# Optimization experiments

Measured on AMD Instinct MI355X. Metric: run time of the kernel, lower is better.

Reference implementation:

```python
import jax, jax.numpy as jnp
import numpy as np

N = 200000   # num nodes
E = 2500000  # num edges
H = 32       # hidden_dim
EPS = 1e-5   # BatchNorm eps


def _gcn_conv(x, W, b, src, dst, norm):
    # GCNConv: D^{-1/2}(A+I)D^{-1/2} X W + b  (self-loops folded in via norm^2 term)
    h = x @ W                                   # [N, H_out]
    coef = norm[src] * norm[dst]                # [E]
    msg = h[src] * coef[:, None]                # [E, H_out] -- dominant HBM traffic
    agg = jax.ops.segment_sum(msg, dst, num_segments=N)
    agg = agg + h * (norm * norm)[:, None]      # self-loop contribution
    return agg + b


def _bn(x, gamma, beta):
    # BatchNorm1d in training mode: batch statistics over the node dimension
    m = jnp.mean(x, axis=0)
    v = jnp.var(x, axis=0)
    return gamma * (x - m) * jax.lax.rsqrt(v + EPS) + beta


def setup_inputs() -> dict:
    key = jax.random.key(0)
    ks = jax.random.split(key, 12)
    x = jax.random.uniform(ks[0], (N, 1), dtype=jnp.float32) * 50.0  # degree-like feature
    edge_index = jax.random.randint(ks[1], (2, E), 0, N, dtype=jnp.int64)
    edge_attr = jax.random.normal(ks[2], (E,), dtype=jnp.float32)
    s = 0.1
    return {
        'x': x, 'edge_index': edge_index, 'edge_attr': edge_attr,
        'W1': jax.random.normal(ks[3], (1, H), dtype=jnp.float32) * s,
        'b1': jnp.zeros((H,), jnp.float32),
        'g1': jnp.ones((H,), jnp.float32), 'be1': jnp.zeros((H,), jnp.float32),
        'W2': jax.random.normal(ks[4], (H, H), dtype=jnp.float32) * s,
        'b2': jnp.zeros((H,), jnp.float32),
        'g2': jnp.ones((H,), jnp.float32), 'be2': jnp.zeros((H,), jnp.float32),
        'W3': jax.random.normal(ks[5], (H, H), dtype=jnp.float32) * s,
        'b3': jnp.zeros((H,), jnp.float32),
        'g3': jnp.ones((H,), jnp.float32), 'be3': jnp.zeros((H,), jnp.float32),
        'fcW': jax.random.normal(ks[6], (H, 1), dtype=jnp.float32) * s,
        'fcb': jnp.zeros((1,), jnp.float32),
    }


def reference(x, edge_index, edge_attr, W1, b1, g1, be1, W2, b2, g2, be2,
              W3, b3, g3, be3, fcW, fcb):
    src, dst = edge_index[0], edge_index[1]
    # symmetric normalization from degrees of A + I
    deg = jax.ops.segment_sum(jnp.ones((E,), x.dtype), dst, num_segments=N) + 1.0
    norm = jax.lax.rsqrt(deg)                   # deg^{-1/2}, [N]

    h = jax.nn.relu(_bn(_gcn_conv(x, W1, b1, src, dst, norm), g1, be1))
    h = jax.nn.relu(_bn(_gcn_conv(h, W2, b2, src, dst, norm), g2, be2))
    h = jax.nn.relu(_bn(_gcn_conv(h, W3, b3, src, dst, norm), g3, be3))
    # dropout is identity in eval / deterministic reference
    return h @ fcW + fcb                        # [N, 1]
```

## Files before the change

### kernel.cpp

```cpp
#include <hip/hip_runtime.h>
#include <hip/hip_bf16.h>
#include <hip/hip_fp16.h>

#define N_NODES 200000
#define N_EDGES 2500000
#define HID 32
#define BN_EPS 1e-5f

#define BKT_SHIFT 10
#define B_BKT ((N_NODES + 1023) / 1024)
#define PAD 16
#define CAPB 14336
#define EDGES_PER_BLK 8192
#define NB_SCAT ((N_EDGES + EDGES_PER_BLK - 1) / EDGES_PER_BLK)

#define SBANK 4096
#define SSTR 16
#define S1SUM 0
#define S1SQ  16
#define L2SUM 32
#define L2SQ  544
#define L3SUM 1056
#define L3SQ  1568

#define NBN32 6250
#define NBH   3125

typedef float nfloat4 __attribute__((ext_vector_type(4)));

__device__ __forceinline__ void atomAddF(float* p, float v) {
    unsafeAtomicAdd(p, v);
}

__device__ __forceinline__ void ntStore4(float* p, float a, float b, float c, float d) {
    nfloat4 v = {a, b, c, d};
    __builtin_nontemporal_store(v, (nfloat4*)p);
}

__global__ void k_init(int* __restrict__ bcur16, float* __restrict__ stats) {
    int i = blockIdx.x * blockDim.x + threadIdx.x;
    if (i < B_BKT * PAD) bcur16[i] = 0;
    if (i < 4 * SBANK) stats[i] = 0.0f;
}

__global__ void __launch_bounds__(1024)
k_scatter(const int* __restrict__ ei, int* __restrict__ bcur16,
          unsigned int* __restrict__ ebuf) {
    __shared__ int lh[B_BKT], lbase[B_BKT], lc[B_BKT];
    int t = threadIdx.x;
    if (t < B_BKT) { lh[t] = 0; lc[t] = 0; }
    __syncthreads();
    int base = blockIdx.x * EDGES_PER_BLK;
    int sv[8], dv[8];
#pragma unroll
    for (int k = 0; k < 8; k++) {
        int e = base + k * 1024 + t;
        if (e < N_EDGES) {
            sv[k] = ei[e];
            dv[k] = ei[N_EDGES + e];
            atomicAdd(&lh[dv[k] >> BKT_SHIFT], 1);
        } else dv[k] = -1;
    }
    __syncthreads();
    if (t < B_BKT) lbase[t] = lh[t] ? atomicAdd(&bcur16[t * PAD], lh[t]) : 0;
    __syncthreads();
#pragma unroll
    for (int k = 0; k < 8; k++) {
        if (dv[k] >= 0) {
            int b = dv[k] >> BKT_SHIFT;
            int loc = atomicAdd(&lc[b], 1);
            ebuf[(size_t)b * CAPB + lbase[b] + loc] =
                ((unsigned)(dv[k] & 1023) << 18) | (unsigned)sv[k];
        }
    }
}

__global__ void __launch_bounds__(1024)
k_bucket(const unsigned int* __restrict__ ebuf, const int* __restrict__ bcur16,
         const float* __restrict__ x, int* __restrict__ rowbeg,
         int* __restrict__ cntg, float* __restrict__ norm,
         float* __restrict__ xp, int* __restrict__ csrc) {
    __shared__ int hist[1024], rbase[1024];
    __shared__ int wsum[16];
    int b = blockIdx.x;
    int t = threadIdx.x;
    int lane = t & 63, wv = t >> 6;
    int count = bcur16[b * PAD];
    size_t ebase = (size_t)b * CAPB;
    int nbase = b << BKT_SHIFT;
    hist[t] = 0;
    __syncthreads();
    for (int i = t; i < count; i += 1024)
        atomicAdd(&hist[ebuf[ebase + i] >> 18], 1);
    __syncthreads();
    int v = hist[t];
    int val = v;
#pragma unroll
    for (int off = 1; off < 64; off <<= 1) {
        int nn = __shfl_up(val, off);
        if (lane >= off) val += nn;
    }
    if (lane == 63) wsum[wv] = val;
    __syncthreads();
    if (t < 16) {
        int wval = wsum[t];
        int wincl = wval;
#pragma unroll
        for (int off = 1; off < 16; off <<= 1) {
            int nn = __shfl_up(wincl, off, 16);
            if (t >= off) wincl += nn;
        }
        wsum[t] = wincl - wval;
    }
    __syncthreads();
    int excl = (val - v) + wsum[wv];
    int rb = b * CAPB + excl;
    rbase[t] = rb;
    int n = nbase + t;
    if (n < N_NODES) {
        rowbeg[n] = rb;
        cntg[n] = v;
        float nm = rsqrtf((float)v + 1.0f);
        norm[n] = nm;
        xp[n] = x[n] * nm;
    }
    __syncthreads();
    hist[t] = 0;
    __syncthreads();
    for (int i = t; i < count; i += 1024) {
        unsigned int w = ebuf[ebase + i];
        int ld = w >> 18;
        int loc = atomicAdd(&hist[ld], 1);
        csrc[rbase[ld] + loc] = (int)(w & 0x3FFFFu);
    }
}

__global__ void __launch_bounds__(256)
k_gather1(const int* __restrict__ rowbeg, const int* __restrict__ cntg,
          const int* __restrict__ csrc, const float* __restrict__ xp,
          const float* __restrict__ norm, float2* __restrict__ sn2,
          float* __restrict__ stats) {
    __shared__ float ls[256], lq[256];
    int tid = threadIdx.x;
    int nl = tid >> 3, q = tid & 7;
    int n = blockIdx.x * 32 + nl;
    int beg = rowbeg[n], dg = cntg[n];
    float A0 = 0.f, A1 = 0.f;
    int i = q;
    for (; i + 8 < dg; i += 16) {
        A0 += xp[__builtin_nontemporal_load(csrc + beg + i)];
        A1 += xp[__builtin_nontemporal_load(csrc + beg + i + 8)];
    }
    if (i < dg) A0 += xp[__builtin_nontemporal_load(csrc + beg + i)];
    float acc = A0 + A1;
    acc += __shfl_xor(acc, 1);
    acc += __shfl_xor(acc, 2);
    acc += __shfl_xor(acc, 4);
    float val = 0.f;
    if (q == 0) {
        acc += xp[n];
        float nm = norm[n];
        val = nm * acc;
        sn2[n] = make_float2(val, nm);
    }
    ls[tid] = val; lq[tid] = val * val;
    __syncthreads();
    for (int off = 128; off; off >>= 1) {
        if (tid < (unsigned)off) { ls[tid] += ls[tid + off]; lq[tid] += lq[tid + off]; }
        __syncthreads();
    }
    if (tid == 0) {
        int bo = (blockIdx.x & 3) * SBANK;
        atomAddF(&stats[bo + S1SUM], ls[0]);
        atomAddF(&stats[bo + S1SQ],  lq[0]);
    }
}

__global__ void __launch_bounds__(256)
k_layer2(const int* __restrict__ rowbeg, const int* __restrict__ cntg,
         const int* __restrict__ csrc, const float2* __restrict__ sn2,
         const float* __restrict__ stats, const float* __restrict__ W1,
         const float* __restrict__ g1, const float* __restrict__ be1,
         const float* __restrict__ W2, float* __restrict__ B,
         float* __restrict__ sumO, float* __restrict__ sqO) {
    __shared__ float w2s[1024];
    __shared__ __align__(16) float ajs[32], bjs[32];
    __shared__ float yx[32][36];
    __shared__ float red[4][8][8];
    int tid = threadIdx.x;
    for (int i = tid; i < 1024; i += 256) w2s[i] = W2[i];
    if (tid < 32) {
        float sm = stats[S1SUM] + stats[SBANK + S1SUM] +
                   stats[2*SBANK + S1SUM] + stats[3*SBANK + S1SUM];
        float sq = stats[S1SQ] + stats[SBANK + S1SQ] +
                   stats[2*SBANK + S1SQ] + stats[3*SBANK + S1SQ];
        float m   = sm * (1.0f / N_NODES);
        float var = sq * (1.0f / N_NODES) - m * m;
        float w = W1[tid];
        float a = g1[tid] * w * rsqrtf(var * w * w + BN_EPS);
        ajs[tid] = a;
        bjs[tid] = be1[tid] - m * a;
    }
    __syncthreads();
    int nl = tid >> 3, l = tid & 7, cg = l * 4;
    int n = blockIdx.x * 32 + nl;
    int dg = cntg[n];
    int beg = rowbeg[n];
    float2 self = sn2[n];
    float nm = self.y;
    float h[32];
#pragma unroll
    for (int k = 0; k < 32; k++) h[k] = 0.f;
    if (l == 0) {
#pragma unroll
        for (int k4 = 0; k4 < 32; k4 += 4) {
            float4 a4 = *(const float4*)&ajs[k4];
            float4 b4 = *(const float4*)&bjs[k4];
            h[k4+0] = nm * fmaxf(fmaf(a4.x, self.x, b4.x), 0.f);
            h[k4+1] = nm * fmaxf(fmaf(a4.y, self.x, b4.y), 0.f);
            h[k4+2] = nm * fmaxf(fmaf(a4.z, self.x, b4.z), 0.f);
            h[k4+3] = nm * fmaxf(fmaf(a4.w, self.x, b4.w), 0.f);
        }
    }
    for (int i = l; i < dg; i += 8) {
        float2 p = sn2[__builtin_nontemporal_load(csrc + beg + i)];
        float w = p.y;
#pragma unroll
        for (int k4 = 0; k4 < 32; k4 += 4) {
            float4 a4 = *(const float4*)&ajs[k4];
            float4 b4 = *(const float4*)&bjs[k4];
            h[k4+0] = fmaf(fmaxf(fmaf(a4.x, p.x, b4.x), 0.f), w, h[k4+0]);
            h[k4+1] = fmaf(fmaxf(fmaf(a4.y, p.x, b4.y), 0.f), w, h[k4+1]);
            h[k4+2] = fmaf(fmaxf(fmaf(a4.z, p.x, b4.z), 0.f), w, h[k4+2]);
            h[k4+3] = fmaf(fmaxf(fmaf(a4.w, p.x, b4.w), 0.f), w, h[k4+3]);
        }
    }
#pragma unroll
    for (int k = 0; k < 32; k++) {
        h[k] += __shfl_xor(h[k], 1);
        h[k] += __shfl_xor(h[k], 2);
        h[k] += __shfl_xor(h[k], 4);
    }
    *(float4*)&yx[nl][cg] = make_float4(h[cg], h[cg+1], h[cg+2], h[cg+3]);
    __syncthreads();
    float o0=0,o1=0,o2=0,o3=0;
#pragma unroll
    for (int k = 0; k < 32; k += 4) {
        float4 hh  = *(const float4*)&yx[nl][k];
        float4 wr0 = *(const float4*)&w2s[(k+0)*32 + cg];
        float4 wr1 = *(const float4*)&w2s[(k+1)*32 + cg];
        float4 wr2 = *(const float4*)&w2s[(k+2)*32 + cg];
        float4 wr3 = *(const float4*)&w2s[(k+3)*32 + cg];
        o0 = fmaf(hh.x,wr0.x, fmaf(hh.y,wr1.x, fmaf(hh.z,wr2.x, fmaf(hh.w,wr3.x, o0))));
        o1 = fmaf(hh.x,wr0.y, fmaf(hh.y,wr1.y, fmaf(hh.z,wr2.y, fmaf(hh.w,wr3.y, o1))));
        o2 = fmaf(hh.x,wr0.z, fmaf(hh.y,wr1.z, fmaf(hh.z,wr2.z, fmaf(hh.w,wr3.z, o2))));
        o3 = fmaf(hh.x,wr0.w, fmaf(hh.y,wr1.w, fmaf(hh.z,wr2.w, fmaf(hh.w,wr3.w, o3))));
    }
    o0 *= nm; o1 *= nm; o2 *= nm; o3 *= nm;
    ntStore4(B + (size_t)n * 32 + cg, o0, o1, o2, o3);
    float s0 = o0, s1 = o1, s2 = o2, s3 = o3;
    float q0 = o0*o0, q1 = o1*o1, q2 = o2*o2, q3 = o3*o3;
#pragma unroll
    for (int mask = 32; mask >= 8; mask >>= 1) {
        s0 += __shfl_xor(s0, mask); s1 += __shfl_xor(s1, mask);
        s2 += __shfl_xor(s2, mask); s3 += __shfl_xor(s3, mask);
        q0 += __shfl_xor(q0, mask); q1 += __shfl_xor(q1, mask);
        q2 += __shfl_xor(q2, mask); q3 += __shfl_xor(q3, mask);
    }
    int wv = tid >> 6, ln = tid & 63;
    if (ln < 8) {
        float* r = red[wv][ln];
        r[0]=s0; r[1]=s1; r[2]=s2; r[3]=s3;
        r[4]=q0; r[5]=q1; r[6]=q2; r[7]=q3;
    }
    __syncthreads();
    if (tid < 8) {
        float tacc[8] = {0,0,0,0,0,0,0,0};
#pragma unroll
        for (int w = 0; w < 4; w++)
#pragma unroll
            for (int k = 0; k < 8; k++) tacc[k] += red[w][tid][k];
        int cb = tid * 4;
        int bo = (blockIdx.x & 3) * SBANK;
#pragma unroll
        for (int k = 0; k < 4; k++) {
            atomAddF(&sumO[bo + (cb + k) * SSTR], tacc[k]);
            atomAddF(&sqO [bo + (cb + k) * SSTR], tacc[4 + k]);
        }
    }
}

__global__ void __launch_bounds__(256)
k_fusedB(const float* __restrict__ norm, const float* __restrict__ sum,
         const float* __restrict__ sumsq, const float* __restrict__ g,
         const float* __restrict__ be, const float* __restrict__ W,
         const float* __restrict__ aggIn, __half* __restrict__ hOut) {
    __shared__ float wl[1024];
    __shared__ float scs[32], shs[32];
    __shared__ float yx[32][36];
    int tid = threadIdx.x;
    for (int i = tid; i < 1024; i += 256) wl[i] = W[i];
    if (tid < 32) {
        int o = tid * SSTR;
        float sm = sum[o] + sum[o+SBANK] + sum[o+2*SBANK] + sum[o+3*SBANK];
        float sq = sumsq[o] + sumsq[o+SBANK] + sumsq[o+2*SBANK] + sumsq[o+3*SBANK];
        float m   = sm * (1.0f / N_NODES);
        float var = sq * (1.0f / N_NODES) - m * m;
        float scj = g[tid] * rsqrtf(var + BN_EPS);
        scs[tid] = scj;
        shs[tid] = be[tid] - m * scj;
    }
    __syncthreads();
    int nl = tid >> 3, cg = (tid & 7) * 4;
    int n = blockIdx.x * 32 + nl;
    float4 bi = *(const float4*)(aggIn + (size_t)n * 32 + cg);
    float y0 = fmaxf(scs[cg  ]*bi.x + shs[cg  ], 0.f);
    float y1 = fmaxf(scs[cg+1]*bi.y + shs[cg+1], 0.f);
    float y2 = fmaxf(scs[cg+2]*bi.z + shs[cg+2], 0.f);
    float y3 = fmaxf(scs[cg+3]*bi.w + shs[cg+3], 0.f);
    *(float4*)&yx[nl][cg] = make_float4(y0,y1,y2,y3);
    __syncthreads();
    float o0=0,o1=0,o2=0,o3=0;
#pragma unroll
    for (int k = 0; k < 32; k += 4) {
        float4 hh  = *(const float4*)&yx[nl][k];
        float4 wr0 = *(const float4*)&wl[(k+0)*32 + cg];
        float4 wr1 = *(const float4*)&wl[(k+1)*32 + cg];
        float4 wr2 = *(const float4*)&wl[(k+2)*32 + cg];
        float4 wr3 = *(const float4*)&wl[(k+3)*32 + cg];
        o0 = fmaf(hh.x,wr0.x, fmaf(hh.y,wr1.x, fmaf(hh.z,wr2.x, fmaf(hh.w,wr3.x, o0))));
        o1 = fmaf(hh.x,wr0.y, fmaf(hh.y,wr1.y, fmaf(hh.z,wr2.y, fmaf(hh.w,wr3.y, o1))));
        o2 = fmaf(hh.x,wr0.z, fmaf(hh.y,wr1.z, fmaf(hh.z,wr2.z, fmaf(hh.w,wr3.z, o2))));
        o3 = fmaf(hh.x,wr0.w, fmaf(hh.y,wr1.w, fmaf(hh.z,wr2.w, fmaf(hh.w,wr3.w, o3))));
    }
    float nm = norm[n];
    __half2 ha = __floats2half2_rn(o0 * nm, o1 * nm);
    __half2 hb = __floats2half2_rn(o2 * nm, o3 * nm);
    float2 pk;
    ((__half2*)&pk)[0] = ha;
    ((__half2*)&pk)[1] = hb;
    *(float2*)(hOut + (size_t)n * 32 + cg) = pk;
}

__device__ __forceinline__ void acc8(float* a, float4 raw) {
    const __half2* h = (const __half2*)&raw;
    float2 f0 = __half22float2(h[0]);
    float2 f1 = __half22float2(h[1]);
    float2 f2 = __half22float2(h[2]);
    float2 f3 = __half22float2(h[3]);
    a[0] += f0.x; a[1] += f0.y; a[2] += f1.x; a[3] += f1.y;
    a[4] += f2.x; a[5] += f2.y; a[6] += f3.x; a[7] += f3.y;
}

__device__ __forceinline__ void acc8m(float* a, float4 raw, float m) {
    const __half2* h = (const __half2*)&raw;
    float2 f0 = __half22float2(h[0]);
    float2 f1 = __half22float2(h[1]);
    float2 f2 = __half22float2(h[2]);
    float2 f3 = __half22float2(h[3]);
    a[0] = fmaf(m, f0.x, a[0]); a[1] = fmaf(m, f0.y, a[1]);
    a[2] = fmaf(m, f1.x, a[2]); a[3] = fmaf(m, f1.y, a[3]);
    a[4] = fmaf(m, f2.x, a[4]); a[5] = fmaf(m, f2.y, a[5]);
    a[6] = fmaf(m, f3.x, a[6]); a[7] = fmaf(m, f3.y, a[7]);
}

__global__ void __launch_bounds__(256)
k_gatherH(const int* __restrict__ rowbeg, const int* __restrict__ cntg,
          const int* __restrict__ csrc, const __half* __restrict__ A,
          const float* __restrict__ norm, float* __restrict__ B,
          float* __restrict__ sum, float* __restrict__ sumsq) {
    int tid = threadIdx.x;
    int nl = tid >> 2;
    int c8 = (tid & 3) * 8;
    int n = blockIdx.x * 64 + nl;
    int beg = rowbeg[n], dg = cntg[n];
    const __half* Ac = A + c8;
    float acc[8] = {0,0,0,0,0,0,0,0};
    acc8(acc, *(const float4*)(Ac + (size_t)n * 32));
    int iters = (dg + 7) >> 3;
    for (int t = 0; t < iters; t++) {
        int i0 = t * 8;
        int e[8]; float m[8];
#pragma unroll
        for (int j = 0; j < 8; j++) {
            int idx = i0 + j;
            bool ok = idx < dg;
            int ic = ok ? idx : dg - 1;
            e[j] = __builtin_nontemporal_load(csrc + beg + ic);
            m[j] = ok ? 1.f : 0.f;
        }
        float4 r0 = *(const float4*)(Ac + (size_t)e[0] * 32);
        float4 r1 = *(const float4*)(Ac + (size_t)e[1] * 32);
        float4 r2 = *(const float4*)(Ac + (size_t)e[2] * 32);
        float4 r3 = *(const float4*)(Ac + (size_t)e[3] * 32);
        float4 r4 = *(const float4*)(Ac + (size_t)e[4] * 32);
        float4 r5 = *(const float4*)(Ac + (size_t)e[5] * 32);
        float4 r6 = *(const float4*)(Ac + (size_t)e[6] * 32);
        float4 r7 = *(const float4*)(Ac + (size_t)e[7] * 32);
        acc8m(acc, r0, m[0]); acc8m(acc, r1, m[1]);
        acc8m(acc, r2, m[2]); acc8m(acc, r3, m[3]);
        acc8m(acc, r4, m[4]); acc8m(acc, r5, m[5]);
        acc8m(acc, r6, m[6]); acc8m(acc, r7, m[7]);
    }
    float nm = norm[n];
    float o[8];
#pragma unroll
    for (int k = 0; k < 8; k++) o[k] = acc[k] * nm;
    ntStore4(B + (size_t)n * 32 + c8,     o[0], o[1], o[2], o[3]);
    ntStore4(B + (size_t)n * 32 + c8 + 4, o[4], o[5], o[6], o[7]);
    float st[16];
#pragma unroll
    for (int k = 0; k < 8; k++) { st[k] = o[k]; st[8 + k] = o[k] * o[k]; }
#pragma unroll
    for (int mask = 32; mask >= 4; mask >>= 1)
#pragma unroll
        for (int k = 0; k < 16; k++) st[k] += __shfl_xor(st[k], mask);
    __shared__ float red[4][4][16];
    int wv = tid >> 6, ln = tid & 63;
    if (ln < 4) {
#pragma unroll
        for (int k = 0; k < 16; k++) red[wv][ln][k] = st[k];
    }
    __syncthreads();
    if (tid < 4) {
        float tacc[16];
#pragma unroll
        for (int k = 0; k < 16; k++) tacc[k] = 0.f;
#pragma unroll
        for (int w = 0; w < 4; w++)
#pragma unroll
            for (int k = 0; k < 16; k++) tacc[k] += red[w][tid][k];
        int cb = tid * 8;
        int bo = (blockIdx.x & 3) * SBANK;
#pragma unroll
        for (int k = 0; k < 8; k++) {
            atomAddF(&sum[bo + (cb + k) * SSTR], tacc[k]);
            atomAddF(&sumsq[bo + (cb + k) * SSTR], tacc[8 + k]);
        }
    }
}

__global__ void __launch_bounds__(256)
k_final(const float* __restrict__ aggIn, const float* __restrict__ sum,
        const float* __restrict__ sumsq, const float* __restrict__ g,
        const float* __restrict__ be, const float* __restrict__ fcW,
        const float* __restrict__ fcb, float* __restrict__ out) {
    __shared__ float scs[32], shs[32], fws[32];
    int tid = threadIdx.x;
    if (tid < 32) {
        int o = tid * SSTR;
        float sm = sum[o] + sum[o+SBANK] + sum[o+2*SBANK] + sum[o+3*SBANK];
        float sq = sumsq[o] + sumsq[o+SBANK] + sumsq[o+2*SBANK] + sumsq[o+3*SBANK];
        float m   = sm * (1.0f / N_NODES);
        float var = sq * (1.0f / N_NODES) - m * m;
        float scj = g[tid] * rsqrtf(var + BN_EPS);
        scs[tid] = scj;
        shs[tid] = be[tid] - m * scj;
        fws[tid] = fcW[tid];
    }
    __syncthreads();
    int nl = tid >> 3, cg = (tid & 7) * 4;
    int n = blockIdx.x * 32 + nl;
    float4 bi = *(const float4*)(aggIn + (size_t)n * 32 + cg);
    float v = fmaxf(scs[cg  ]*bi.x + shs[cg  ], 0.f) * fws[cg  ]
            + fmaxf(scs[cg+1]*bi.y + shs[cg+1], 0.f) * fws[cg+1]
            + fmaxf(scs[cg+2]*bi.z + shs[cg+2], 0.f) * fws[cg+2]
            + fmaxf(scs[cg+3]*bi.w + shs[cg+3], 0.f) * fws[cg+3];
    v += __shfl_xor(v, 1);
    v += __shfl_xor(v, 2);
    v += __shfl_xor(v, 4);
    if ((tid & 7) == 0) out[n] = v + fcb[0];
}

extern "C" void kernel_launch(void* const* d_in, const int* in_sizes, int n_in,
                              void* d_out, int out_size, void* d_ws, size_t ws_size,
                              hipStream_t stream) {
    const float* x   = (const float*)d_in[0];
    const int*   ei  = (const int*)d_in[1];
    const float* W1  = (const float*)d_in[3];
    const float* g1  = (const float*)d_in[5];
    const float* be1 = (const float*)d_in[6];
    const float* W2  = (const float*)d_in[7];
    const float* g2  = (const float*)d_in[9];
    const float* be2 = (const float*)d_in[10];
    const float* W3  = (const float*)d_in[11];
    const float* g3  = (const float*)d_in[13];
    const float* be3 = (const float*)d_in[14];
    const float* fcW = (const float*)d_in[15];
    const float* fcb = (const float*)d_in[16];
    float* out = (float*)d_out;

    char* base = (char*)d_ws;
    __half*       A16  = (__half*)base;
    unsigned int* ebuf = (unsigned int*)base;
    float*  B      = (float*)(base + (size_t)N_NODES * 32 * 4);
    int*    csrc   = (int*)(base + (size_t)N_NODES * 32 * 8);
    int*    rowbeg = csrc + (size_t)B_BKT * CAPB;
    int*    cntg   = rowbeg + N_NODES;
    float*  norm   = (float*)(cntg + N_NODES);
    float*  xp     = norm + N_NODES;
    float2* sn2    = (float2*)(xp + N_NODES);
    float*  stats  = (float*)(sn2 + N_NODES);
    int*    bcur16 = (int*)(stats + 4 * SBANK);

    k_init   <<<64, 256, 0, stream>>>(bcur16, stats);
    k_scatter<<<NB_SCAT, 1024, 0, stream>>>(ei, bcur16, ebuf);
    k_bucket <<<B_BKT, 1024, 0, stream>>>(ebuf, bcur16, x, rowbeg, cntg, norm, xp, csrc);
    k_gather1<<<NBN32, 256, 0, stream>>>(rowbeg, cntg, csrc, xp, norm, sn2, stats);
    k_layer2 <<<NBN32, 256, 0, stream>>>(rowbeg, cntg, csrc, sn2, stats,
                                         W1, g1, be1, W2, B,
                                         stats + L2SUM, stats + L2SQ);
    k_fusedB <<<NBN32, 256, 0, stream>>>(norm, stats + L2SUM, stats + L2SQ,
                                         g2, be2, W3, B, A16);
    k_gatherH<<<NBH, 256, 0, stream>>>(rowbeg, cntg, csrc, A16, norm, B,
                                       stats + L3SUM, stats + L3SQ);
    k_final  <<<NBN32, 256, 0, stream>>>(B, stats + L3SUM, stats + L3SQ,
                                         g3, be3, fcW, fcb, out);
}
```

Measured before the change: 346.0 us.

## Split layer-2 gather by channel instead of by edge, removing shuffle reduction

The layer-2 aggregation changes from each of 8 lanes handling a strided subset of edges for all 32 channels (then reducing with 96 shuffles) to each lane handling all edges for its own 4 channels. Each lane loads 8 edge indices and their sn2 entries per iteration. This drops the 32-register accumulator array and the cross-lane shuffle reduction, which should lower register pressure and ALU work. In exchange, every lane of the group now loads the same indices and sn2 values redundantly (broadcast loads), and the compute per lane is 4 channels times every edge.

```diff
diff --git a/kernel.cpp b/kernel.cpp
--- a/kernel.cpp
+++ b/kernel.cpp
@@ -175,6 +175,8 @@
         atomAddF(&stats[bo + S1SQ],  lq[0]);
     }
 }
+
+#define PHI(aa, bb, pp) ((pp).y * fmaxf(fmaf((aa), (pp).x, (bb)), 0.f))
 
 __global__ void __launch_bounds__(256)
 k_layer2(const int* __restrict__ rowbeg, const int* __restrict__ cntg,
@@ -202,46 +204,38 @@
         bjs[tid] = be1[tid] - m * a;
     }
     __syncthreads();
-    int nl = tid >> 3, l = tid & 7, cg = l * 4;
+    int nl = tid >> 3, cg = (tid & 7) * 4;
     int n = blockIdx.x * 32 + nl;
     int dg = cntg[n];
     int beg = rowbeg[n];
+    float a0 = ajs[cg], a1 = ajs[cg+1], a2 = ajs[cg+2], a3 = ajs[cg+3];
+    float b0 = bjs[cg], b1 = bjs[cg+1], b2 = bjs[cg+2], b3 = bjs[cg+3];
     float2 self = sn2[n];
     float nm = self.y;
-    float h[32];
-#pragma unroll
-    for (int k = 0; k < 32; k++) h[k] = 0.f;
-    if (l == 0) {
-#pragma unroll
-        for (int k4 = 0; k4 < 32; k4 += 4) {
-            float4 a4 = *(const float4*)&ajs[k4];
-            float4 b4 = *(const float4*)&bjs[k4];
-            h[k4+0] = nm * fmaxf(fmaf(a4.x, self.x, b4.x), 0.f);
-            h[k4+1] = nm * fmaxf(fmaf(a4.y, self.x, b4.y), 0.f);
-            h[k4+2] = nm * fmaxf(fmaf(a4.z, self.x, b4.z), 0.f);
-            h[k4+3] = nm * fmaxf(fmaf(a4.w, self.x, b4.w), 0.f);
-        }
-    }
-    for (int i = l; i < dg; i += 8) {
-        float2 p = sn2[__builtin_nontemporal_load(csrc + beg + i)];
-        float w = p.y;
-#pragma unroll
-        for (int k4 = 0; k4 < 32; k4 += 4) {
-            float4 a4 = *(const float4*)&ajs[k4];
-            float4 b4 = *(const float4*)&bjs[k4];
-            h[k4+0] = fmaf(fmaxf(fmaf(a4.x, p.x, b4.x), 0.f), w, h[k4+0]);
-            h[k4+1] = fmaf(fmaxf(fmaf(a4.y, p.x, b4.y), 0.f), w, h[k4+1]);
-            h[k4+2] = fmaf(fmaxf(fmaf(a4.z, p.x, b4.z), 0.f), w, h[k4+2]);
-            h[k4+3] = fmaf(fmaxf(fmaf(a4.w, p.x, b4.w), 0.f), w, h[k4+3]);
-        }
-    }
-#pragma unroll
-    for (int k = 0; k < 32; k++) {
-        h[k] += __shfl_xor(h[k], 1);
-        h[k] += __shfl_xor(h[k], 2);
-        h[k] += __shfl_xor(h[k], 4);
-    }
-    *(float4*)&yx[nl][cg] = make_float4(h[cg], h[cg+1], h[cg+2], h[cg+3]);
+    float h0 = PHI(a0,b0,self), h1 = PHI(a1,b1,self),
+          h2 = PHI(a2,b2,self), h3 = PHI(a3,b3,self);
+    int iters = (dg + 7) >> 3;
+    for (int t = 0; t < iters; t++) {
+        int i0 = t * 8;
+        int e[8];
+#pragma unroll
+        for (int j = 0; j < 8; j++) {
+            int idx = i0 + j;
+            e[j] = __builtin_nontemporal_load(csrc + beg + (idx < dg ? idx : 0));
+        }
+        float2 p[8];
+#pragma unroll
+        for (int j = 0; j < 8; j++) p[j] = sn2[e[j]];
+#pragma unroll
+        for (int j = 0; j < 8; j++) {
+            float w = (i0 + j < dg) ? p[j].y : 0.f;
+            h0 = fmaf(fmaxf(fmaf(a0, p[j].x, b0), 0.f), w, h0);
+            h1 = fmaf(fmaxf(fmaf(a1, p[j].x, b1), 0.f), w, h1);
+            h2 = fmaf(fmaxf(fmaf(a2, p[j].x, b2), 0.f), w, h2);
+            h3 = fmaf(fmaxf(fmaf(a3, p[j].x, b3), 0.f), w, h3);
+        }
+    }
+    *(float4*)&yx[nl][cg] = make_float4(h0, h1, h2, h3);
     __syncthreads();
     float o0=0,o1=0,o2=0,o3=0;
 #pragma unroll
```

New measurement: 336.2 us. 1.03x faster.
